# Kernel tuning notes

Measured on AMD Instinct MI355X. Metric: run time of the kernel, lower is better.

Reference implementation:

```python
import jax, jax.numpy as jnp
import numpy as np

N_NODES = 100000
N_EDGES = 1600000
HIDDEN = 64


def setup_inputs() -> dict:
    key = jax.random.key(0)
    ks = jax.random.split(key, 10)
    s = 0.1
    x = jax.random.normal(ks[0], (N_NODES, 1), dtype=jnp.float32)
    edge_index = jax.random.randint(ks[1], (2, N_EDGES), 0, N_NODES, dtype=jnp.int32)
    edge_weight = jnp.ones((N_EDGES,), dtype=jnp.float32)
    f32 = jnp.float32
    return {
        "x": x,
        "edge_weight": edge_weight,
        "Wz": jax.random.normal(ks[2], (1, HIDDEN), f32) * s,
        "bz": jnp.zeros((HIDDEN,), f32),
        "Lz": jax.random.normal(ks[3], (2 * HIDDEN, HIDDEN), f32) * s,
        "lbz": jnp.zeros((HIDDEN,), f32),
        "Wr": jax.random.normal(ks[4], (1, HIDDEN), f32) * s,
        "br": jnp.zeros((HIDDEN,), f32),
        "Lr": jax.random.normal(ks[5], (2 * HIDDEN, HIDDEN), f32) * s,
        "lbr": jnp.zeros((HIDDEN,), f32),
        "Wh": jax.random.normal(ks[6], (1, HIDDEN), f32) * s,
        "bh": jnp.zeros((HIDDEN,), f32),
        "Lh": jax.random.normal(ks[7], (2 * HIDDEN, HIDDEN), f32) * s,
        "lbh": jnp.zeros((HIDDEN,), f32),
        "Wout": jax.random.normal(ks[8], (HIDDEN, 1), f32) * s,
        "bout": jnp.zeros((1,), f32),
        "edge_index": edge_index,
    }


def reference(x, edge_weight, Wz, bz, Lz, lbz, Wr, br, Lr, lbr,
              Wh, bh, Lh, lbh, Wout, bout, edge_index):
    N = x.shape[0]
    hidden = Wz.shape[1]
    src, dst = edge_index[0], edge_index[1]
    # GCN normalization with added self-loops (PyG gcn_norm)
    loop = jnp.arange(N, dtype=src.dtype)
    src2 = jnp.concatenate([src, loop])
    dst2 = jnp.concatenate([dst, loop])
    ew2 = jnp.concatenate([edge_weight, jnp.ones((N,), x.dtype)])
    deg = jax.ops.segment_sum(ew2, dst2, num_segments=N)  # [N]
    dinv = jnp.where(deg > 0, jax.lax.rsqrt(deg), 0.0)
    norm = dinv[src2] * ew2 * dinv[dst2]  # [E+N]

    def gcn(W, b):
        xw = x @ W  # [N, H]
        agg = jax.ops.segment_sum(xw[src2] * norm[:, None], dst2, num_segments=N)
        return agg + b

    # TGCN cell with H0 = 0 (no hidden state passed)
    H = jnp.zeros((N, hidden), x.dtype)
    Z = jax.nn.sigmoid(jnp.concatenate([gcn(Wz, bz), H], axis=1) @ Lz + lbz)
    R = jax.nn.sigmoid(jnp.concatenate([gcn(Wr, br), H], axis=1) @ Lr + lbr)
    Ht = jnp.tanh(jnp.concatenate([gcn(Wh, bh), H * R], axis=1) @ Lh + lbh)
    Hn = Z * H + (1.0 - Z) * Ht
    h = jax.nn.relu(Hn)
    return h @ Wout + bout
```

## Files before the change

### kernel.cpp

```cpp
#include <hip/hip_runtime.h>
#include <math.h>

#define HIDDEN 64
#define RANGE 16384
#define G_CHUNKS 32

template <bool WEIGHTED>
__global__ __launch_bounds__(1024)
void k_bin(const int* __restrict__ dst, const int* __restrict__ src,
           const float* __restrict__ ew, const float* __restrict__ w,
           float* __restrict__ partials, int N, int E, int nranges) {
    __shared__ float bins[RANGE];
    const int r = blockIdx.x % nranges;
    const int c = blockIdx.x / nranges;
    const int base = r * RANGE;
    const unsigned rsize = (unsigned)min(RANGE, N - base);

    float4* b4 = (float4*)bins;
    for (int i = threadIdx.x; i < RANGE / 4; i += blockDim.x)
        b4[i] = make_float4(0.f, 0.f, 0.f, 0.f);
    __syncthreads();

    long long e0 = (((long long)E * c) / G_CHUNKS) & ~3LL;
    long long e1 = (c == G_CHUNKS - 1) ? (long long)E
                                       : ((((long long)E * (c + 1)) / G_CHUNKS) & ~3LL);
    const int nvec = (int)((e1 - e0) >> 2);
    const int4*   dst4 = (const int4*)(dst + e0);
    const float4* ew4  = (const float4*)(ew + e0);
    const int4*   src4 = (const int4*)(src + e0);

    for (int i = threadIdx.x; i < nvec; i += blockDim.x) {
        int4   d = dst4[i];
        float4 t = ew4[i];
        if (WEIGHTED) {
            int4 s = src4[i];
            unsigned l0 = (unsigned)(d.x - base);
            unsigned l1 = (unsigned)(d.y - base);
            unsigned l2 = (unsigned)(d.z - base);
            unsigned l3 = (unsigned)(d.w - base);
            if (l0 < rsize) atomicAdd(&bins[l0], w[s.x] * t.x);
            if (l1 < rsize) atomicAdd(&bins[l1], w[s.y] * t.y);
            if (l2 < rsize) atomicAdd(&bins[l2], w[s.z] * t.z);
            if (l3 < rsize) atomicAdd(&bins[l3], w[s.w] * t.w);
        } else {
            unsigned l0 = (unsigned)(d.x - base);
            unsigned l1 = (unsigned)(d.y - base);
            unsigned l2 = (unsigned)(d.z - base);
            unsigned l3 = (unsigned)(d.w - base);
            if (l0 < rsize) atomicAdd(&bins[l0], t.x);
            if (l1 < rsize) atomicAdd(&bins[l1], t.y);
            if (l2 < rsize) atomicAdd(&bins[l2], t.z);
            if (l3 < rsize) atomicAdd(&bins[l3], t.w);
        }
    }
    for (long long e = e0 + ((long long)nvec << 2) + threadIdx.x; e < e1; e += blockDim.x) {
        unsigned l = (unsigned)(dst[e] - base);
        if (l < rsize) {
            float v = WEIGHTED ? w[src[e]] * ew[e] : ew[e];
            atomicAdd(&bins[l], v);
        }
    }
    __syncthreads();

    float4* outp = (float4*)(partials + ((size_t)c * nranges + r) * RANGE);
    for (int i = threadIdx.x; i < RANGE / 4; i += blockDim.x) outp[i] = b4[i];
}

__global__ void k_node(const float* __restrict__ x, const float* __restrict__ partials,
                       float* __restrict__ dinv, float* __restrict__ w,
                       int N, int nranges,
                       const float* __restrict__ Wz, const float* __restrict__ bz,
                       const float* __restrict__ Lz, const float* __restrict__ lbz,
                       const float* __restrict__ Wh, const float* __restrict__ bh,
                       const float* __restrict__ Lh, const float* __restrict__ lbh,
                       float* __restrict__ coeff) {
    int i = blockIdx.x * blockDim.x + threadIdx.x;
    if (i < N) {
        int r = i / RANGE, local = i % RANGE;
        const float* p = partials + (size_t)r * RANGE + local;
        float d = 1.0f;
        #pragma unroll
        for (int c = 0; c < G_CHUNKS; ++c)
            d += p[(size_t)c * nranges * RANGE];
        float di = rsqrtf(d);
        dinv[i] = di;
        w[i] = di * x[i];
    }
    if (blockIdx.x == 0 && threadIdx.x < HIDDEN) {
        int j = threadIdx.x;
        float vz = 0.f, cz = 0.f, vh = 0.f, ch = 0.f;
        for (int k = 0; k < HIDDEN; ++k) {
            float lz = Lz[k * HIDDEN + j];
            float lh = Lh[k * HIDDEN + j];
            vz += Wz[k] * lz;
            cz += bz[k] * lz;
            vh += Wh[k] * lh;
            ch += bh[k] * lh;
        }
        coeff[j]       = vz;
        coeff[64 + j]  = cz + lbz[j];
        coeff[128 + j] = vh;
        coeff[192 + j] = ch + lbh[j];
    }
}

__global__ void k_out(const float* __restrict__ partials, const float* __restrict__ dinv,
                      const float* __restrict__ w, const float* __restrict__ coeff,
                      const float* __restrict__ Wout, const float* __restrict__ bout,
                      float* __restrict__ out, int N, int nranges) {
    __shared__ float c[5 * HIDDEN];
    __shared__ float b0;
    if (threadIdx.x < 4 * HIDDEN) c[threadIdx.x] = coeff[threadIdx.x];
    if (threadIdx.x < HIDDEN) c[4 * HIDDEN + threadIdx.x] = Wout[threadIdx.x];
    if (threadIdx.x == 0) b0 = bout[0];
    __syncthreads();
    int i = blockIdx.x * blockDim.x + threadIdx.x;
    if (i < N) {
        int r = i / RANGE, local = i % RANGE;
        const float* p = partials + (size_t)r * RANGE + local;
        float g = w[i];
        #pragma unroll
        for (int k = 0; k < G_CHUNKS; ++k)
            g += p[(size_t)k * nranges * RANGE];
        float si = dinv[i] * g;
        float acc = b0;
        #pragma unroll
        for (int j = 0; j < HIDDEN; ++j) {
            float zp = fminf(fmaxf(si * c[j] + c[64 + j], -30.f), 30.f);
            float hp = fminf(fmaxf(si * c[128 + j] + c[192 + j], -15.f), 15.f);
            float a  = __expf(2.0f * hp);
            float t  = (a - 1.0f) / (a + 1.0f);
            float zn = 1.0f / (1.0f + __expf(zp));
            float hn = zn * t;
            hn = hn > 0.0f ? hn : 0.0f;
            acc = fmaf(hn, c[256 + j], acc);
        }
        out[i] = acc;
    }
}

extern "C" void kernel_launch(void* const* d_in, const int* in_sizes, int n_in,
                              void* d_out, int out_size, void* d_ws, size_t ws_size,
                              hipStream_t stream) {
    const float* x    = (const float*)d_in[0];
    const float* ew   = (const float*)d_in[1];
    const float* Wz   = (const float*)d_in[2];
    const float* bz   = (const float*)d_in[3];
    const float* Lz   = (const float*)d_in[4];
    const float* lbz  = (const float*)d_in[5];
    const float* Wh   = (const float*)d_in[10];
    const float* bh   = (const float*)d_in[11];
    const float* Lh   = (const float*)d_in[12];
    const float* lbh  = (const float*)d_in[13];
    const float* Wout = (const float*)d_in[14];
    const float* bout = (const float*)d_in[15];
    const int*   eidx = (const int*)d_in[16];

    const int N = in_sizes[0];
    const int E = in_sizes[1];
    const int* src = eidx;
    const int* dst = eidx + E;

    const int nranges = (N + RANGE - 1) / RANGE;

    float* partials = (float*)d_ws;
    float* dinv     = partials + (size_t)G_CHUNKS * nranges * RANGE;
    float* w        = dinv + N;
    float* coeff    = w + N;

    const int TB = 256;
    const int grid_bin = G_CHUNKS * nranges;

    k_bin<false><<<grid_bin, 1024, 0, stream>>>(dst, src, ew, (const float*)nullptr,
                                                partials, N, E, nranges);
    k_node<<<(N + TB - 1) / TB, TB, 0, stream>>>(x, partials, dinv, w, N, nranges,
                                                 Wz, bz, Lz, lbz, Wh, bh, Lh, lbh, coeff);
    k_bin<true><<<grid_bin, 1024, 0, stream>>>(dst, src, ew, w,
                                               partials, N, E, nranges);
    k_out<<<(N + TB - 1) / TB, TB, 0, stream>>>(partials, dinv, w, coeff, Wout, bout,
                                                (float*)d_out, N, nranges);
}
```

Measured before the change: 159.3 us.

## Pre-bucket edges by destination range with histogram, scan, and scatter

Adds a counting-sort pass (histogram, scan, scatter) that groups edges by destination node range and packs local dst and src into one word. Each binning block then reads only the edges for its own range instead of every block scanning its whole chunk and discarding out-of-range entries. This is meant to cut the roughly nranges-fold redundant edge reads in both binning passes. The cost is three extra kernel launches, a global atomic-based scatter of all edges, and extra workspace for the packed arrays. Packing assumes fewer than 2^17 nodes.

```diff
diff --git a/kernel.cpp b/kernel.cpp
--- a/kernel.cpp
+++ b/kernel.cpp
@@ -3,62 +3,98 @@
 
 #define HIDDEN 64
 #define RANGE 16384
-#define G_CHUNKS 32
+#define RSHIFT 14
+#define G 32
+#define NSEG 256
+#define MAXR 8
+
+
+__global__ void k_hist(const int* __restrict__ dst, int* __restrict__ counts,
+                       int E, int nranges) {
+    __shared__ int h[MAXR];
+    if (threadIdx.x < MAXR) h[threadIdx.x] = 0;
+    __syncthreads();
+    int e0 = (int)((long long)E * blockIdx.x / NSEG);
+    int e1 = (int)((long long)E * (blockIdx.x + 1) / NSEG);
+    for (int e = e0 + threadIdx.x; e < e1; e += blockDim.x)
+        atomicAdd(&h[dst[e] >> RSHIFT], 1);
+    __syncthreads();
+    if (threadIdx.x < MAXR) counts[blockIdx.x * MAXR + threadIdx.x] = h[threadIdx.x];
+}
+
+__global__ __launch_bounds__(NSEG) void k_scan(const int* __restrict__ counts,
+                                               int* __restrict__ offs,
+                                               int* __restrict__ bbase) {
+    __shared__ int sh[NSEG][MAXR];
+    __shared__ int base[MAXR + 1];
+    int t = threadIdx.x;
+    int own[MAXR];
+    #pragma unroll
+    for (int b = 0; b < MAXR; ++b) { own[b] = counts[t * MAXR + b]; sh[t][b] = own[b]; }
+    __syncthreads();
+    for (int step = 1; step < NSEG; step <<= 1) {
+        int v[MAXR];
+        if (t >= step) {
+            #pragma unroll
+            for (int b = 0; b < MAXR; ++b) v[b] = sh[t - step][b];
+        }
+        __syncthreads();
+        if (t >= step) {
+            #pragma unroll
+            for (int b = 0; b < MAXR; ++b) sh[t][b] += v[b];
+        }
+        __syncthreads();
+    }
+    if (t == 0) {
+        int a = 0;
+        #pragma unroll
+        for (int b = 0; b < MAXR; ++b) { base[b] = a; a += sh[NSEG - 1][b]; }
+        base[MAXR] = a;
+    }
+    __syncthreads();
+    #pragma unroll
+    for (int b = 0; b < MAXR; ++b) offs[t * MAXR + b] = base[b] + sh[t][b] - own[b];
+    if (t < MAXR + 1) bbase[t] = base[t];
+}
+
+__global__ void k_scatter(const int* __restrict__ dst, const int* __restrict__ src,
+                          const float* __restrict__ ew, const int* __restrict__ offs,
+                          unsigned* __restrict__ spack, float* __restrict__ sew, int E) {
+    __shared__ int cur[MAXR];
+    if (threadIdx.x < MAXR) cur[threadIdx.x] = offs[blockIdx.x * MAXR + threadIdx.x];
+    __syncthreads();
+    int e0 = (int)((long long)E * blockIdx.x / NSEG);
+    int e1 = (int)((long long)E * (blockIdx.x + 1) / NSEG);
+    for (int e = e0 + threadIdx.x; e < e1; e += blockDim.x) {
+        int d = dst[e];
+        int pos = atomicAdd(&cur[d >> RSHIFT], 1);
+        spack[pos] = ((unsigned)(d & (RANGE - 1)) << 17) | (unsigned)src[e];
+        sew[pos] = ew[e];
+    }
+}
 
 template <bool WEIGHTED>
 __global__ __launch_bounds__(1024)
-void k_bin(const int* __restrict__ dst, const int* __restrict__ src,
-           const float* __restrict__ ew, const float* __restrict__ w,
-           float* __restrict__ partials, int N, int E, int nranges) {
+void k_bin(const unsigned* __restrict__ spack, const float* __restrict__ sew,
+           const float* __restrict__ w, const int* __restrict__ bbase,
+           float* __restrict__ partials, int nranges) {
     __shared__ float bins[RANGE];
-    const int r = blockIdx.x % nranges;
-    const int c = blockIdx.x / nranges;
-    const int base = r * RANGE;
-    const unsigned rsize = (unsigned)min(RANGE, N - base);
-
     float4* b4 = (float4*)bins;
     for (int i = threadIdx.x; i < RANGE / 4; i += blockDim.x)
         b4[i] = make_float4(0.f, 0.f, 0.f, 0.f);
     __syncthreads();
 
-    long long e0 = (((long long)E * c) / G_CHUNKS) & ~3LL;
-    long long e1 = (c == G_CHUNKS - 1) ? (long long)E
-                                       : ((((long long)E * (c + 1)) / G_CHUNKS) & ~3LL);
-    const int nvec = (int)((e1 - e0) >> 2);
-    const int4*   dst4 = (const int4*)(dst + e0);
-    const float4* ew4  = (const float4*)(ew + e0);
-    const int4*   src4 = (const int4*)(src + e0);
-
-    for (int i = threadIdx.x; i < nvec; i += blockDim.x) {
-        int4   d = dst4[i];
-        float4 t = ew4[i];
-        if (WEIGHTED) {
-            int4 s = src4[i];
-            unsigned l0 = (unsigned)(d.x - base);
-            unsigned l1 = (unsigned)(d.y - base);
-            unsigned l2 = (unsigned)(d.z - base);
-            unsigned l3 = (unsigned)(d.w - base);
-            if (l0 < rsize) atomicAdd(&bins[l0], w[s.x] * t.x);
-            if (l1 < rsize) atomicAdd(&bins[l1], w[s.y] * t.y);
-            if (l2 < rsize) atomicAdd(&bins[l2], w[s.z] * t.z);
-            if (l3 < rsize) atomicAdd(&bins[l3], w[s.w] * t.w);
-        } else {
-            unsigned l0 = (unsigned)(d.x - base);
-            unsigned l1 = (unsigned)(d.y - base);
-            unsigned l2 = (unsigned)(d.z - base);
-            unsigned l3 = (unsigned)(d.w - base);
-            if (l0 < rsize) atomicAdd(&bins[l0], t.x);
-            if (l1 < rsize) atomicAdd(&bins[l1], t.y);
-            if (l2 < rsize) atomicAdd(&bins[l2], t.z);
-            if (l3 < rsize) atomicAdd(&bins[l3], t.w);
-        }
-    }
-    for (long long e = e0 + ((long long)nvec << 2) + threadIdx.x; e < e1; e += blockDim.x) {
-        unsigned l = (unsigned)(dst[e] - base);
-        if (l < rsize) {
-            float v = WEIGHTED ? w[src[e]] * ew[e] : ew[e];
-            atomicAdd(&bins[l], v);
-        }
+    const int r = blockIdx.x / G, c = blockIdx.x % G;
+    const int s = bbase[r];
+    const int len = bbase[r + 1] - s;
+    const int a0 = s + (int)((long long)len * c / G);
+    const int a1 = s + (int)((long long)len * (c + 1) / G);
+
+    for (int e = a0 + threadIdx.x; e < a1; e += blockDim.x) {
+        unsigned p = spack[e];
+        float v = sew[e];
+        if (WEIGHTED) v *= w[p & 0x1FFFFu];
+        atomicAdd(&bins[p >> 17], v);
     }
     __syncthreads();
 
@@ -76,12 +112,11 @@
                        float* __restrict__ coeff) {
     int i = blockIdx.x * blockDim.x + threadIdx.x;
     if (i < N) {
-        int r = i / RANGE, local = i % RANGE;
+        int r = i >> RSHIFT, local = i & (RANGE - 1);
         const float* p = partials + (size_t)r * RANGE + local;
         float d = 1.0f;
         #pragma unroll
-        for (int c = 0; c < G_CHUNKS; ++c)
-            d += p[(size_t)c * nranges * RANGE];
+        for (int c = 0; c < G; ++c) d += p[(size_t)c * nranges * RANGE];
         float di = rsqrtf(d);
         dinv[i] = di;
         w[i] = di * x[i];
@@ -116,12 +151,11 @@
     __syncthreads();
     int i = blockIdx.x * blockDim.x + threadIdx.x;
     if (i < N) {
-        int r = i / RANGE, local = i % RANGE;
+        int r = i >> RSHIFT, local = i & (RANGE - 1);
         const float* p = partials + (size_t)r * RANGE + local;
         float g = w[i];
         #pragma unroll
-        for (int k = 0; k < G_CHUNKS; ++k)
-            g += p[(size_t)k * nranges * RANGE];
+        for (int k = 0; k < G; ++k) g += p[(size_t)k * nranges * RANGE];
         float si = dinv[i] * g;
         float acc = b0;
         #pragma unroll
@@ -163,20 +197,28 @@
 
     const int nranges = (N + RANGE - 1) / RANGE;
 
-    float* partials = (float*)d_ws;
-    float* dinv     = partials + (size_t)G_CHUNKS * nranges * RANGE;
-    float* w        = dinv + N;
-    float* coeff    = w + N;
+    float*    partials = (float*)d_ws;
+    unsigned* spack    = (unsigned*)(partials + (size_t)G * nranges * RANGE);
+    float*    sew      = (float*)(spack + E);
+    float*    dinv     = sew + E;
+    float*    w        = dinv + N;
+    float*    coeff    = w + N;
+    int*      counts   = (int*)(coeff + 4 * HIDDEN);
+    int*      offs     = counts + NSEG * MAXR;
+    int*      bbase    = offs + NSEG * MAXR;
 
     const int TB = 256;
-    const int grid_bin = G_CHUNKS * nranges;
-
-    k_bin<false><<<grid_bin, 1024, 0, stream>>>(dst, src, ew, (const float*)nullptr,
-                                                partials, N, E, nranges);
+    const int grid_bin = nranges * G;
+
+    k_hist<<<NSEG, TB, 0, stream>>>(dst, counts, E, nranges);
+    k_scan<<<1, NSEG, 0, stream>>>(counts, offs, bbase);
+    k_scatter<<<NSEG, TB, 0, stream>>>(dst, src, ew, offs, spack, sew, E);
+
+    k_bin<false><<<grid_bin, 1024, 0, stream>>>(spack, sew, (const float*)nullptr,
+                                                bbase, partials, nranges);
     k_node<<<(N + TB - 1) / TB, TB, 0, stream>>>(x, partials, dinv, w, N, nranges,
                                                  Wz, bz, Lz, lbz, Wh, bh, Lh, lbh, coeff);
-    k_bin<true><<<grid_bin, 1024, 0, stream>>>(dst, src, ew, w,
-                                               partials, N, E, nranges);
+    k_bin<true><<<grid_bin, 1024, 0, stream>>>(spack, sew, w, bbase, partials, nranges);
     k_out<<<(N + TB - 1) / TB, TB, 0, stream>>>(partials, dinv, w, coeff, Wout, bout,
                                                 (float*)d_out, N, nranges);
 }
```

New measurement: 174.7 us. 9.7% more time.

## Compact per-range edge lists in first binning pass to avoid full rescan

Applied to the files above, without the earlier changes.

During the degree-binning pass, each range block now also writes the edges it owns into a per-(range, chunk) slice. Each entry packs the local destination and source index into one word, plus the weight, and slot positions come from wave ballot and a shared-memory cursor. The weighted aggregation pass then reads only its own compacted edges instead of rescanning every edge for every range. Block-to-(range, chunk) mapping is also reordered so that neighbouring blocks share edge chunks. The cost is extra src reads, global writes and wave-level atomics in the first pass, and a packing scheme that only holds while node indices fit in 17 bits.

```diff
diff --git a/kernel.cpp b/kernel.cpp
--- a/kernel.cpp
+++ b/kernel.cpp
@@ -3,67 +3,84 @@
 
 #define HIDDEN 64
 #define RANGE 16384
-#define G_CHUNKS 32
-
-template <bool WEIGHTED>
+#define RSHIFT 14
+#define G 32
+#define PACK_SHIFT 17
+
+__device__ __forceinline__ void map_rc(int b, int nranges, int& r, int& c) {
+    int x = b & 7;
+    int rest = b >> 3;
+    r = rest % nranges;
+    c = x + 8 * (rest / nranges);
+}
+
 __global__ __launch_bounds__(1024)
-void k_bin(const int* __restrict__ dst, const int* __restrict__ src,
-           const float* __restrict__ ew, const float* __restrict__ w,
-           float* __restrict__ partials, int N, int E, int nranges) {
+void k_binA(const int* __restrict__ dst, const int* __restrict__ src,
+            const float* __restrict__ ew, float* __restrict__ partials,
+            uint2* __restrict__ comp, int* __restrict__ counts,
+            int N, int E, int nranges, int cap) {
     __shared__ float bins[RANGE];
-    const int r = blockIdx.x % nranges;
-    const int c = blockIdx.x / nranges;
-    const int base = r * RANGE;
-    const unsigned rsize = (unsigned)min(RANGE, N - base);
-
+    __shared__ int cursor;
     float4* b4 = (float4*)bins;
     for (int i = threadIdx.x; i < RANGE / 4; i += blockDim.x)
         b4[i] = make_float4(0.f, 0.f, 0.f, 0.f);
-    __syncthreads();
-
-    long long e0 = (((long long)E * c) / G_CHUNKS) & ~3LL;
-    long long e1 = (c == G_CHUNKS - 1) ? (long long)E
-                                       : ((((long long)E * (c + 1)) / G_CHUNKS) & ~3LL);
+    if (threadIdx.x == 0) cursor = 0;
+    __syncthreads();
+
+    int r, c;
+    map_rc(blockIdx.x, nranges, r, c);
+    const int base = r * RANGE;
+    const unsigned rsize = (unsigned)min(RANGE, N - base);
+    uint2* slice = comp + (size_t)(r * G + c) * cap;
+
+    long long e0 = (((long long)E * c) / G) & ~3LL;
+    long long e1 = (c == G - 1) ? (long long)E
+                                : ((((long long)E * (c + 1)) / G) & ~3LL);
     const int nvec = (int)((e1 - e0) >> 2);
     const int4*   dst4 = (const int4*)(dst + e0);
+    const int4*   src4 = (const int4*)(src + e0);
     const float4* ew4  = (const float4*)(ew + e0);
-    const int4*   src4 = (const int4*)(src + e0);
+    const int lane = threadIdx.x & 63;
 
     for (int i = threadIdx.x; i < nvec; i += blockDim.x) {
         int4   d = dst4[i];
+        int4   s = src4[i];
         float4 t = ew4[i];
-        if (WEIGHTED) {
-            int4 s = src4[i];
-            unsigned l0 = (unsigned)(d.x - base);
-            unsigned l1 = (unsigned)(d.y - base);
-            unsigned l2 = (unsigned)(d.z - base);
-            unsigned l3 = (unsigned)(d.w - base);
-            if (l0 < rsize) atomicAdd(&bins[l0], w[s.x] * t.x);
-            if (l1 < rsize) atomicAdd(&bins[l1], w[s.y] * t.y);
-            if (l2 < rsize) atomicAdd(&bins[l2], w[s.z] * t.z);
-            if (l3 < rsize) atomicAdd(&bins[l3], w[s.w] * t.w);
-        } else {
-            unsigned l0 = (unsigned)(d.x - base);
-            unsigned l1 = (unsigned)(d.y - base);
-            unsigned l2 = (unsigned)(d.z - base);
-            unsigned l3 = (unsigned)(d.w - base);
-            if (l0 < rsize) atomicAdd(&bins[l0], t.x);
-            if (l1 < rsize) atomicAdd(&bins[l1], t.y);
-            if (l2 < rsize) atomicAdd(&bins[l2], t.z);
-            if (l3 < rsize) atomicAdd(&bins[l3], t.w);
+        int   dd[4] = {d.x, d.y, d.z, d.w};
+        int   ss[4] = {s.x, s.y, s.z, s.w};
+        float tt[4] = {t.x, t.y, t.z, t.w};
+        #pragma unroll
+        for (int j = 0; j < 4; ++j) {
+            unsigned l = (unsigned)(dd[j] - base);
+            bool p = l < rsize;
+            if (p) atomicAdd(&bins[l], tt[j]);
+            unsigned long long m = __ballot(p);
+            if (m) {
+                int leader = __ffsll((unsigned long long)m) - 1;
+                int pre = __popcll(m & ((1ULL << lane) - 1ULL));
+                int bpos = 0;
+                if (lane == leader) bpos = atomicAdd(&cursor, __popcll(m));
+                bpos = __shfl(bpos, leader);
+                if (p) slice[bpos + pre] =
+                    make_uint2((l << PACK_SHIFT) | (unsigned)ss[j],
+                               __float_as_uint(tt[j]));
+            }
         }
     }
     for (long long e = e0 + ((long long)nvec << 2) + threadIdx.x; e < e1; e += blockDim.x) {
         unsigned l = (unsigned)(dst[e] - base);
         if (l < rsize) {
-            float v = WEIGHTED ? w[src[e]] * ew[e] : ew[e];
-            atomicAdd(&bins[l], v);
+            atomicAdd(&bins[l], ew[e]);
+            int bpos = atomicAdd(&cursor, 1);
+            slice[bpos] = make_uint2((l << PACK_SHIFT) | (unsigned)src[e],
+                                     __float_as_uint(ew[e]));
         }
     }
     __syncthreads();
 
     float4* outp = (float4*)(partials + ((size_t)c * nranges + r) * RANGE);
     for (int i = threadIdx.x; i < RANGE / 4; i += blockDim.x) outp[i] = b4[i];
+    if (threadIdx.x == 0) counts[r * G + c] = cursor;
 }
 
 __global__ void k_node(const float* __restrict__ x, const float* __restrict__ partials,
@@ -76,12 +93,11 @@
                        float* __restrict__ coeff) {
     int i = blockIdx.x * blockDim.x + threadIdx.x;
     if (i < N) {
-        int r = i / RANGE, local = i % RANGE;
+        int r = i >> RSHIFT, local = i & (RANGE - 1);
         const float* p = partials + (size_t)r * RANGE + local;
         float d = 1.0f;
         #pragma unroll
-        for (int c = 0; c < G_CHUNKS; ++c)
-            d += p[(size_t)c * nranges * RANGE];
+        for (int c = 0; c < G; ++c) d += p[(size_t)c * nranges * RANGE];
         float di = rsqrtf(d);
         dinv[i] = di;
         w[i] = di * x[i];
@@ -104,6 +120,32 @@
     }
 }
 
+__global__ __launch_bounds__(1024)
+void k_binB(const uint2* __restrict__ comp, const int* __restrict__ counts,
+            const float* __restrict__ w, float* __restrict__ partials,
+            int nranges, int cap) {
+    __shared__ float bins[RANGE];
+    float4* b4 = (float4*)bins;
+    for (int i = threadIdx.x; i < RANGE / 4; i += blockDim.x)
+        b4[i] = make_float4(0.f, 0.f, 0.f, 0.f);
+    __syncthreads();
+
+    int r, c;
+    map_rc(blockIdx.x, nranges, r, c);
+    const uint2* slice = comp + (size_t)(r * G + c) * cap;
+    const int n = counts[r * G + c];
+
+    for (int i = threadIdx.x; i < n; i += blockDim.x) {
+        uint2 e = slice[i];
+        float v = w[e.x & ((1u << PACK_SHIFT) - 1u)] * __uint_as_float(e.y);
+        atomicAdd(&bins[e.x >> PACK_SHIFT], v);
+    }
+    __syncthreads();
+
+    float4* outp = (float4*)(partials + ((size_t)c * nranges + r) * RANGE);
+    for (int i = threadIdx.x; i < RANGE / 4; i += blockDim.x) outp[i] = b4[i];
+}
+
 __global__ void k_out(const float* __restrict__ partials, const float* __restrict__ dinv,
                       const float* __restrict__ w, const float* __restrict__ coeff,
                       const float* __restrict__ Wout, const float* __restrict__ bout,
@@ -116,12 +158,11 @@
     __syncthreads();
     int i = blockIdx.x * blockDim.x + threadIdx.x;
     if (i < N) {
-        int r = i / RANGE, local = i % RANGE;
+        int r = i >> RSHIFT, local = i & (RANGE - 1);
         const float* p = partials + (size_t)r * RANGE + local;
         float g = w[i];
         #pragma unroll
-        for (int k = 0; k < G_CHUNKS; ++k)
-            g += p[(size_t)k * nranges * RANGE];
+        for (int k = 0; k < G; ++k) g += p[(size_t)k * nranges * RANGE];
         float si = dinv[i] * g;
         float acc = b0;
         #pragma unroll
@@ -162,21 +203,23 @@
     const int* dst = eidx + E;
 
     const int nranges = (N + RANGE - 1) / RANGE;
+    const int cap = (((E + G - 1) / G) + 15) & ~3;
 
     float* partials = (float*)d_ws;
-    float* dinv     = partials + (size_t)G_CHUNKS * nranges * RANGE;
+    uint2* comp     = (uint2*)(partials + (size_t)G * nranges * RANGE);
+    float* dinv     = (float*)(comp + (size_t)nranges * G * cap);
     float* w        = dinv + N;
     float* coeff    = w + N;
+    int*   counts   = (int*)(coeff + 4 * HIDDEN);
 
     const int TB = 256;
-    const int grid_bin = G_CHUNKS * nranges;
-
-    k_bin<false><<<grid_bin, 1024, 0, stream>>>(dst, src, ew, (const float*)nullptr,
-                                                partials, N, E, nranges);
+    const int grid_bin = nranges * G;
+
+    k_binA<<<grid_bin, 1024, 0, stream>>>(dst, src, ew, partials, comp, counts,
+                                          N, E, nranges, cap);
     k_node<<<(N + TB - 1) / TB, TB, 0, stream>>>(x, partials, dinv, w, N, nranges,
                                                  Wz, bz, Lz, lbz, Wh, bh, Lh, lbh, coeff);
-    k_bin<true><<<grid_bin, 1024, 0, stream>>>(dst, src, ew, w,
-                                               partials, N, E, nranges);
+    k_binB<<<grid_bin, 1024, 0, stream>>>(comp, counts, w, partials, nranges, cap);
     k_out<<<(N + TB - 1) / TB, TB, 0, stream>>>(partials, dinv, w, coeff, Wout, bout,
                                                 (float*)d_out, N, nranges);
 }
```

Measured after the change: 154.8 us. -2.8%, faster.
